# Kernel tuning notes

Measured on AMD Instinct MI355X. Metric: run time of the kernel, lower is better.

## Reference

```python
import jax, jax.numpy as jnp
import numpy as np
from jax import lax

T_STEPS = 40
BATCH = 2048
UNITS = 1024
INPUT_DIM = 1024
Q_BASIS = 8
ORDER = 4  # skfda BSpline default (cubic)


def bspline_basis(ts, q, k=ORDER):
    """Cox-de Boor B-spline basis, n_basis=q, order k, domain [0,1]. ts: (T,) -> (T,q)."""
    ts = np.asarray(ts, dtype=np.float64)
    breaks = np.linspace(0.0, 1.0, q - k + 2)
    knots = np.concatenate([np.zeros(k - 1), breaks, np.ones(k - 1)])  # len q+k
    n0 = len(knots) - 1
    N = np.zeros((len(ts), n0))
    for i in range(n0):
        N[:, i] = ((ts >= knots[i]) & (ts < knots[i + 1])).astype(np.float64)
    for d in range(1, k):
        Nn = np.zeros((len(ts), n0 - d))
        for i in range(n0 - d):
            out = np.zeros(len(ts))
            den1 = knots[i + d] - knots[i]
            if den1 > 0:
                out += (ts - knots[i]) / den1 * N[:, i]
            den2 = knots[i + d + 1] - knots[i + 1]
            if den2 > 0:
                out += (knots[i + d + 1] - ts) / den2 * N[:, i + 1]
            Nn[:, i] = out
        N = Nn
    # at right endpoint t==1 only the last basis is nonzero (value 1)
    at_end = ts >= 1.0 - 1e-12
    N[at_end] = 0.0
    N[at_end, -1] = 1.0
    return N.astype(np.float32)


def setup_inputs() -> dict:
    key = jax.random.key(0)
    k1, k2, k3 = jax.random.split(key, 3)
    D = UNITS + INPUT_DIM
    x = jax.random.normal(k1, (BATCH, T_STEPS, INPUT_DIM), dtype=jnp.float32)
    h0 = jnp.zeros((BATCH, UNITS), dtype=jnp.float32)
    Qw = jax.random.normal(k2, (D, Q_BASIS * UNITS), dtype=jnp.float32) / np.sqrt(D)
    bias = jax.random.uniform(k3, (UNITS,), dtype=jnp.float32, minval=-0.05, maxval=0.05)
    Bt_all = jnp.asarray(bspline_basis(np.linspace(0.0, 1.0, T_STEPS), Q_BASIS))
    return {"x": x, "h0": h0, "Qw": Qw, "bias": bias, "Bt_all": Bt_all}


def reference(x, h0, Qw, bias, Bt_all):
    B, T, I = x.shape
    U = h0.shape[-1]
    q = Bt_all.shape[-1]
    D = Qw.shape[0]
    # block_diag(Bt,...,Bt).T contraction == reshape Q to (D, U, q) and contract q with Bt
    Qr = Qw.reshape(D, U, q)
    W_all = jnp.einsum('duq,tq->tdu', Qr, Bt_all)  # (T, D, U) per-step weight matrices

    def step(h, xw):
        x_t, W_t = xw                       # (B,I), (D,U)
        cat = jnp.concatenate([h, x_t], axis=-1)  # (B, U+I) = (B, D); state first, as in cell
        h_new = jnp.tanh(cat @ W_t + bias)
        return h_new, h_new

    xs = jnp.swapaxes(x, 0, 1)              # (T, B, I)
    _, hs = lax.scan(step, h0, (xs, W_all))
    return jnp.swapaxes(hs, 0, 1)           # (B, T, U)
```

## Files before the change

### kernel.cpp

```cpp
#include <hip/hip_runtime.h>
#include <hip/hip_fp16.h>

#define TS 40
#define NB 2048
#define NU 1024
#define NI 1024
#define ND 2048
#define UD (1024 * 2048)

typedef _Float16 half8 __attribute__((ext_vector_type(8)));
typedef _Float16 half4v __attribute__((ext_vector_type(4)));
typedef float floatx4 __attribute__((ext_vector_type(4)));

__device__ __forceinline__ float tanh_fast(float v) {
  float e = __expf(2.0f * v);
  return 1.0f - 2.0f / (e + 1.0f);
}

__device__ __forceinline__ void gload16(const void* g, void* l) {
  __builtin_amdgcn_global_load_lds(
      (const __attribute__((address_space(1))) void*)g,
      (__attribute__((address_space(3))) void*)l, 16, 0, 0);
}

__device__ __forceinline__ int tile_off(int r, int c8) {
  return (((((r >> 4) * 2 + (c8 >> 2)) << 6) + ((c8 & 3) << 4) + (r & 15)) << 4);
}


__global__ __launch_bounds__(256) void prep_all(
    const float* __restrict__ Qw, const float* __restrict__ Bt,
    _Float16* __restrict__ W,
    const float* __restrict__ x, _Float16* __restrict__ X,
    const float* __restrict__ h0, _Float16* __restrict__ hb)
{
  __shared__ char shm[66816];
  const int tid = threadIdx.x;
  const int bid = blockIdx.x;

  if (bid < 512) {
    _Float16* ldsQ = (_Float16*)shm;
    float* ldsB = (float*)(shm + 65536);
    const int kt = bid & 31;
    const int ut = bid >> 5;
    for (int i = tid; i < TS * 8; i += 256) ldsB[i] = Bt[i];
    const float* qb = Qw + (size_t)(kt * 64) * 8192 + ut * 512;
#pragma unroll
    for (int i = 0; i < 32; ++i) {
      int s = i * 256 + tid;
      int dk = s >> 7, c4 = s & 127;
      float4 v = *(const float4*)(qb + (size_t)dk * 8192 + c4 * 4);
      _Float16* d = &ldsQ[dk * 512 + c4 * 4];
      d[0] = (_Float16)v.x; d[1] = (_Float16)v.y;
      d[2] = (_Float16)v.z; d[3] = (_Float16)v.w;
    }
    __syncthreads();
    const int w = tid >> 6, lane = tid & 63;
    const int dur = lane & 7, ko = lane >> 3;
#pragma unroll 1
    for (int sp = 0; sp < 2; ++sp) {
      const int stripe = w * 2 + sp;
      const int du = stripe * 8 + dur;
      float Q[8][8];
#pragma unroll
      for (int j = 0; j < 8; ++j)
#pragma unroll
        for (int q = 0; q < 8; ++q)
          Q[j][q] = (float)ldsQ[(ko * 8 + j) * 512 + du * 8 + q];
      const int obase = tile_off(du, ko);
#pragma unroll 1
      for (int t = 0; t < TS; ++t) {
        float b[8];
#pragma unroll
        for (int q = 0; q < 8; ++q) b[q] = ldsB[t * 8 + q];
        half8 v;
#pragma unroll
        for (int j = 0; j < 8; ++j) {
          float s = 0.f;
#pragma unroll
          for (int q = 0; q < 8; ++q) s += Q[j][q] * b[q];
          v[j] = (_Float16)s;
        }
        size_t tile = ((size_t)t * 16 + ut) * 32 + kt;
        *(half8*)((char*)W + tile * 8192 + obase) = v;
      }
    }
  } else if (bid < 1792) {
    char* stage = shm;
    const int b2 = bid - 512;
    const int bt = b2 & 31, t = b2 >> 5;
    char* outb = (char*)X + ((size_t)(t * 32 + bt) * 16) * 8192;
    const int r = tid >> 2, cq = tid & 3;
#pragma unroll 1
    for (int kt = 0; kt < 16; ++kt) {
      const float* src =
          x + (size_t)(bt * 64 + r) * (TS * NI) + (size_t)t * NI + kt * 64 + cq * 16;
      float4 a0 = *(const float4*)(src);
      float4 a1 = *(const float4*)(src + 4);
      float4 a2 = *(const float4*)(src + 8);
      float4 a3 = *(const float4*)(src + 12);
      half8 h0v, h1v;
      h0v[0] = (_Float16)a0.x; h0v[1] = (_Float16)a0.y;
      h0v[2] = (_Float16)a0.z; h0v[3] = (_Float16)a0.w;
      h0v[4] = (_Float16)a1.x; h0v[5] = (_Float16)a1.y;
      h0v[6] = (_Float16)a1.z; h0v[7] = (_Float16)a1.w;
      h1v[0] = (_Float16)a2.x; h1v[1] = (_Float16)a2.y;
      h1v[2] = (_Float16)a2.z; h1v[3] = (_Float16)a2.w;
      h1v[4] = (_Float16)a3.x; h1v[5] = (_Float16)a3.y;
      h1v[6] = (_Float16)a3.z; h1v[7] = (_Float16)a3.w;
      *(half8*)(stage + tile_off(r, cq * 2)) = h0v;
      *(half8*)(stage + tile_off(r, cq * 2 + 1)) = h1v;
      __syncthreads();
      uint4 v0 = *(const uint4*)(stage + tid * 32);
      uint4 v1 = *(const uint4*)(stage + tid * 32 + 16);
      *(uint4*)(outb + (size_t)kt * 8192 + tid * 32) = v0;
      *(uint4*)(outb + (size_t)kt * 8192 + tid * 32 + 16) = v1;
      __syncthreads();
    }
  } else {
    int g = (bid - 1792) * 256 + tid;
    int tile_id = g >> 9, rc = g & 511;
    int bt = tile_id >> 4, kt = tile_id & 15;
    int r = rc >> 3, c8 = rc & 7;
    const float* src = h0 + (size_t)(bt * 64 + r) * NU + kt * 64 + c8 * 8;
    float4 v0 = *(const float4*)src;
    float4 v1 = *(const float4*)(src + 4);
    half8 h;
    h[0] = (_Float16)v0.x; h[1] = (_Float16)v0.y;
    h[2] = (_Float16)v0.z; h[3] = (_Float16)v0.w;
    h[4] = (_Float16)v1.x; h[5] = (_Float16)v1.y;
    h[6] = (_Float16)v1.z; h[7] = (_Float16)v1.w;
    *(half8*)((char*)hb + (size_t)tile_id * 8192 + tile_off(r, c8)) = h;
  }
}

__global__ __launch_bounds__(256) void xproj4(
    const _Float16* __restrict__ X, const _Float16* __restrict__ W,
    const float* __restrict__ bias, _Float16* __restrict__ pre)
{
  __shared__ char lds[65536];
  const int tid = threadIdx.x;
  const int bt2 = blockIdx.x;
  const int ut2 = blockIdx.y;
  const int t   = blockIdx.z;
  const int lane = tid & 63, w = tid >> 6;
  const int wm2 = w >> 1, wn2 = w & 1;
  const int l15 = lane & 15, lk = lane >> 4;

  const char* Xb = (const char*)X + (((size_t)t * 32 + bt2 * 2) * 16) * 8192;
  const char* Wb = (const char*)W + (((size_t)t * 16 + ut2 * 2) * 32 + 16) * 8192;

  float bv[4];
#pragma unroll
  for (int nf = 0; nf < 4; ++nf)
    bv[nf] = bias[ut2 * 128 + wn2 * 64 + nf * 16 + l15];

  auto issue = [&](int p) {
    const char* src = (w < 2)
        ? Xb + (size_t)w * (16 * 8192) + (size_t)p * 8192
        : Wb + (size_t)(w - 2) * (32 * 8192) + (size_t)p * 8192;
    src += lane * 16;
    char* dst = lds + (p & 1) * 32768 + w * 8192;
#pragma unroll
    for (int i = 0; i < 8; ++i) gload16(src + i * 1024, dst + i * 1024);
  };

  floatx4 acc[4][4] = {};

  auto comp = [&](int p) {
    const char* pA = lds + (p & 1) * 32768 + wm2 * 8192;
    const char* pB = lds + (p & 1) * 32768 + 16384 + wn2 * 8192;
    __builtin_amdgcn_s_setprio(1);
#pragma unroll
    for (int kk = 0; kk < 2; ++kk) {
      half8 af[4], bf[4];
#pragma unroll
      for (int mf = 0; mf < 4; ++mf)
        af[mf] = *(const half8*)(pA + ((mf * 2 + kk) << 10) + lane * 16);
#pragma unroll
      for (int nf = 0; nf < 4; ++nf)
        bf[nf] = *(const half8*)(pB + ((nf * 2 + kk) << 10) + lane * 16);
#pragma unroll
      for (int mf = 0; mf < 4; ++mf)
#pragma unroll
        for (int nf = 0; nf < 4; ++nf)
          acc[mf][nf] = __builtin_amdgcn_mfma_f32_16x16x32_f16(
              af[mf], bf[nf], acc[mf][nf], 0, 0, 0);
    }
    __builtin_amdgcn_s_setprio(0);
  };

  issue(0);
#pragma unroll 1
  for (int p = 0; p < 16; ++p) {
    if (p + 1 < 16) {
      issue(p + 1);
      asm volatile("s_waitcnt vmcnt(8)" ::: "memory");
    } else {
      asm volatile("s_waitcnt vmcnt(0)" ::: "memory");
    }
    __builtin_amdgcn_s_barrier();
    comp(p);
    __builtin_amdgcn_s_barrier();
  }

  char* pbase = (char*)pre + (size_t)t * (512 * 8192);
  const int bidS = (bt2 * 2 + wm2) + 32 * (ut2 * 2 + wn2);
#pragma unroll
  for (int k = 0; k < 2; ++k)
#pragma unroll
    for (int nfp = 0; nfp < 4; ++nfp) {
      _Float16 hv[8];
#pragma unroll
      for (int j = 0; j < 4; ++j) {
        hv[j]     = (_Float16)(acc[2 * k][nfp][j] + bv[nfp]);
        hv[4 + j] = (_Float16)(acc[2 * k + 1][nfp][j] + bv[nfp]);
      }
      int wS = k * 4 + nfp;
      char* dst = pbase + ((size_t)bidS * 512 + wS * 64 + lane) * 16;
      *(uint4*)dst = ((const uint4*)hv)[0];
    }
}

__global__ __launch_bounds__(512) void serial6(
    const _Float16* __restrict__ Wh,
    const _Float16* __restrict__ pret,
    const _Float16* __restrict__ hprev,
    _Float16* __restrict__ hnext,
    float* __restrict__ outt)
{
  __shared__ uint4 lds4[4096];
  const int tid = threadIdx.x, bid = blockIdx.x;
  const int bt = bid & 31, ut = bid >> 5;
  const int bidS = bt + 32 * ut;
  const int lane = tid & 63, w = tid >> 6;
  const int wm = w >> 2, wn = w & 3;
  const int l15 = lane & 15, lk = lane >> 4;
  const int b0 = bt * 64, u0 = ut * 64;

  uint4 prv;
  {
    const uint4* pp = (const uint4*)((const char*)pret +
                                     ((size_t)bidS * 512 + tid) * 16);
    prv = pp[0];
  }

  const char* Hb = (const char*)hprev + (size_t)bt * 16 * 8192;
  const char* Wb = (const char*)Wh + (size_t)ut * 32 * 8192;

  auto issue = [&](int kt) {
    char* la = (char*)lds4 + (kt & 3) * 16384 + w * 2048;
    const char* g = (w < 4)
        ? Hb + (size_t)kt * 8192 + w * 2048 + lane * 16
        : Wb + (size_t)kt * 8192 + (w - 4) * 2048 + lane * 16;
    gload16(g, la);
    gload16(g + 1024, la + 1024);
  };

  floatx4 acc[2] = {};

  issue(0);
  issue(1);
  issue(2);
#pragma unroll 1
  for (int p = 0; p < 16; ++p) {
    if (p < 14)       asm volatile("s_waitcnt vmcnt(4)" ::: "memory");
    else if (p == 14) asm volatile("s_waitcnt vmcnt(2)" ::: "memory");
    else              asm volatile("s_waitcnt vmcnt(0)" ::: "memory");
    __builtin_amdgcn_s_barrier();
    if (p + 3 < 16) issue(p + 3);
    const char* pA = (const char*)lds4 + (p & 3) * 16384;
    const char* pB = pA + 8192;
    __builtin_amdgcn_s_setprio(1);
#pragma unroll
    for (int kk = 0; kk < 2; ++kk) {
      half8 af[2], bf;
#pragma unroll
      for (int mf = 0; mf < 2; ++mf)
        af[mf] = *(const half8*)(pA + ((((wm * 2 + mf) * 2 + kk) << 10) + lane * 16));
      bf = *(const half8*)(pB + (((wn * 2 + kk) << 10) + lane * 16));
#pragma unroll
      for (int mf = 0; mf < 2; ++mf)
        acc[mf] = __builtin_amdgcn_mfma_f32_16x16x32_f16(af[mf], bf, acc[mf], 0, 0, 0);
    }
    __builtin_amdgcn_s_setprio(0);
  }

  _Float16 prh[8];
  *(uint4*)&prh[0] = prv;
  {
    int u = u0 + wn * 16 + l15;
#pragma unroll
    for (int mf = 0; mf < 2; ++mf) {
      int brow = b0 + wm * 32 + mf * 16 + (lk << 2);
#pragma unroll
      for (int j = 0; j < 4; ++j) {
        int b = brow + j;
        float p = (float)prh[mf * 4 + j];
        float v = tanh_fast(acc[mf][j] + p);
        outt[(size_t)b * (TS * NU) + u] = v;
        *(_Float16*)((char*)hnext + (((size_t)(bt * 16 + ut)) << 13) +
                     tile_off(b & 63, (u & 63) >> 3) + (u & 7) * 2) = (_Float16)v;
      }
    }
  }
}

__global__ __launch_bounds__(256) void wprep_lin(
    const float* __restrict__ Qw, const float* __restrict__ Bt,
    _Float16* __restrict__ W, int t0, int nt)
{
  __shared__ float ldsQ[32 * 257];
  __shared__ float ldsB[TS * 8];
  const int tid = threadIdx.x;
  const int k0 = blockIdx.x * 32;
  const int u0 = blockIdx.y * 32;
  for (int i = tid; i < TS * 8; i += 256) ldsB[i] = Bt[i];
  const float* qbase = Qw + (size_t)k0 * 8192 + (size_t)u0 * 8;
#pragma unroll
  for (int i = 0; i < 8; ++i) {
    int s = i * 256 + tid;
    int r = s >> 6, c4 = s & 63;
    float4 v = *(const float4*)(qbase + (size_t)r * 8192 + c4 * 4);
    float* d = &ldsQ[r * 257 + c4 * 4];
    d[0] = v.x; d[1] = v.y; d[2] = v.z; d[3] = v.w;
  }
  __syncthreads();
  const int kl = tid & 31;
  const int ug = tid >> 5;
#pragma unroll
  for (int p = 0; p < 4; ++p) {
    int uu = p * 8 + ug;
    float q[8];
#pragma unroll
    for (int j = 0; j < 8; ++j) q[j] = ldsQ[kl * 257 + uu * 8 + j];
    size_t obase = (size_t)(u0 + uu) * 2048 + k0 + kl;
    for (int tt = 0; tt < nt; ++tt) {
      const float* bt = &ldsB[(t0 + tt) * 8];
      float v = 0.f;
#pragma unroll
      for (int j = 0; j < 8; ++j) v += q[j] * bt[j];
      W[(size_t)tt * UD + obase] = (_Float16)v;
    }
  }
}

__global__ __launch_bounds__(256) void step_gemm(
    const float* __restrict__ xt, const float* __restrict__ hp, long hstride,
    const _Float16* __restrict__ Wt, const float* __restrict__ bias,
    float* __restrict__ outt)
{
  __shared__ _Float16 ldsA[2][64 * 64];
  __shared__ _Float16 ldsB[2][128 * 64];
  const int tid = threadIdx.x;
  const int b0 = blockIdx.x * 64;
  const int u0 = blockIdx.y * 128;
  const int lane = tid & 63;
  const int wv = tid >> 6;
  const int wm = wv >> 1, wn = wv & 1;
  const int l15 = lane & 15, lk = lane >> 4;

  float4 areg[4];
  uint4 breg[4];

  auto stage_load = [&](int kt) {
    const int k0 = kt * 64;
    const float* src; size_t stride; int koff;
    if (k0 < NU) { src = hp; stride = (size_t)hstride; koff = k0; }
    else { src = xt; stride = (size_t)TS * NI; koff = k0 - NU; }
#pragma unroll
    for (int i = 0; i < 4; ++i) {
      int s = i * 256 + tid;
      int r = s >> 4, c4 = s & 15;
      areg[i] = *(const float4*)(src + (size_t)(b0 + r) * stride + koff + c4 * 4);
    }
    const _Float16* wsrc = Wt + (size_t)u0 * 2048 + k0;
#pragma unroll
    for (int i = 0; i < 4; ++i) {
      int s = i * 256 + tid;
      int u = s >> 3, c8 = s & 7;
      breg[i] = *(const uint4*)(wsrc + (size_t)u * 2048 + c8 * 8);
    }
  };

  auto stage_write = [&](int buf) {
    char* pA = (char*)&ldsA[buf][0];
    char* pB = (char*)&ldsB[buf][0];
#pragma unroll
    for (int i = 0; i < 4; ++i) {
      int s = i * 256 + tid;
      int r = s >> 4, c4 = s & 15;
      half4v h;
      h[0] = (_Float16)areg[i].x; h[1] = (_Float16)areg[i].y;
      h[2] = (_Float16)areg[i].z; h[3] = (_Float16)areg[i].w;
      int off = (r * 128 + c4 * 8) ^ ((r & 7) << 4);
      *(half4v*)(pA + off) = h;
    }
#pragma unroll
    for (int i = 0; i < 4; ++i) {
      int s = i * 256 + tid;
      int u = s >> 3, c8 = s & 7;
      int off = (u * 128 + c8 * 16) ^ ((u & 7) << 4);
      *(uint4*)(pB + off) = breg[i];
    }
  };

  floatx4 acc[2][4] = {};

  auto compute = [&](int buf) {
    const char* pA = (const char*)&ldsA[buf][0];
    const char* pB = (const char*)&ldsB[buf][0];
#pragma unroll
    for (int kk = 0; kk < 2; ++kk) {
      half8 af[2], bf[4];
#pragma unroll
      for (int mf = 0; mf < 2; ++mf) {
        int r = wm * 32 + mf * 16 + l15;
        int off = r * 128 + ((((kk << 2) | lk) ^ (r & 7)) << 4);
        af[mf] = *(const half8*)(pA + off);
      }
#pragma unroll
      for (int nf = 0; nf < 4; ++nf) {
        int u = wn * 64 + nf * 16 + l15;
        int off = u * 128 + ((((kk << 2) | lk) ^ (u & 7)) << 4);
        bf[nf] = *(const half8*)(pB + off);
      }
#pragma unroll
      for (int mf = 0; mf < 2; ++mf)
#pragma unroll
        for (int nf = 0; nf < 4; ++nf)
          acc[mf][nf] =
              __builtin_amdgcn_mfma_f32_16x16x32_f16(af[mf], bf[nf], acc[mf][nf], 0, 0, 0);
    }
  };

  stage_load(0);
  stage_write(0);
  __syncthreads();
#pragma unroll 1
  for (int kt = 0; kt < 32; ++kt) {
    int cur = kt & 1;
    if (kt + 1 < 32) stage_load(kt + 1);
    compute(cur);
    if (kt + 1 < 32) stage_write(cur ^ 1);
    __syncthreads();
  }

#pragma unroll
  for (int mf = 0; mf < 2; ++mf)
#pragma unroll
    for (int nf = 0; nf < 4; ++nf) {
      int u = u0 + wn * 64 + nf * 16 + l15;
      float bv = bias[u];
      int brow = b0 + wm * 32 + mf * 16 + (lk << 2);
#pragma unroll
      for (int j = 0; j < 4; ++j) {
        float prev = acc[mf][nf][j] + bv;
        outt[(size_t)(brow + j) * (TS * NU) + u] = tanh_fast(prev);
      }
    }
}

extern "C" void kernel_launch(void* const* d_in, const int* in_sizes, int n_in,
                              void* d_out, int out_size, void* d_ws, size_t ws_size,
                              hipStream_t stream) {
  const float* x    = (const float*)d_in[0];
  const float* h0   = (const float*)d_in[1];
  const float* Qw   = (const float*)d_in[2];
  const float* bias = (const float*)d_in[3];
  const float* Bt   = (const float*)d_in[4];
  float* out = (float*)d_out;

  char* ws = (char*)d_ws;
  const size_t w_bytes    = (size_t)UD * TS * sizeof(_Float16);
  const size_t x_bytes    = w_bytes;
  const size_t pre_bytes  = w_bytes;
  const size_t slot_bytes = (size_t)NB * NU * sizeof(_Float16);
  const size_t need = w_bytes + x_bytes + pre_bytes + 2 * slot_bytes;

  if (ws_size >= need) {
    _Float16* W   = (_Float16*)ws;
    _Float16* X   = (_Float16*)(ws + w_bytes);
    _Float16* pre = (_Float16*)(ws + w_bytes + x_bytes);
    _Float16* hb  = (_Float16*)(ws + w_bytes + x_bytes + pre_bytes);
    const size_t SLOT = (size_t)NB * NU;

    prep_all<<<dim3(2816), 256, 0, stream>>>(Qw, Bt, W, x, X, h0, hb);
    xproj4<<<dim3(16, 8, TS), 256, 0, stream>>>(X, W, bias, pre);

    for (int t = 0; t < TS; ++t) {
      const _Float16* hprev = hb + (size_t)(t & 1) * SLOT;
      _Float16* hnext = hb + (size_t)((t + 1) & 1) * SLOT;
      serial6<<<dim3(512), 512, 0, stream>>>(
          W + (size_t)t * UD, pre + (size_t)t * SLOT, hprev, hnext,
          out + (size_t)t * NU);
    }
  } else {
    _Float16* W = (_Float16*)ws;
    const bool big = ws_size >= w_bytes;
    if (big) wprep_lin<<<dim3(64, 32), 256, 0, stream>>>(Qw, Bt, W, 0, TS);
    for (int t = 0; t < TS; ++t) {
      const _Float16* Wtp;
      if (big) {
        Wtp = W + (size_t)t * UD;
      } else {
        wprep_lin<<<dim3(64, 32), 256, 0, stream>>>(Qw, Bt, W, t, 1);
        Wtp = W;
      }
      const float* hp = (t == 0) ? h0 : out + (size_t)(t - 1) * NU;
      long hstride = (t == 0) ? NU : (long)TS * NU;
      step_gemm<<<dim3(32, 8), 256, 0, stream>>>(
          x + (size_t)t * NI, hp, hstride, Wtp, bias, out + (size_t)t * NU);
    }
  }
}
```

Baseline: 922.2 us.

## Replace per-step serial kernel launches with one persistent cooperative kernel using flags

Swaps the 40 per-timestep serial6 launches for a single cooperative persistent kernel, serial7, that loops over time steps. Blocks synchronise through per-batch-tile atomic counters instead of kernel boundaries. Each block prefetches its weight tiles for the next step before spinning on the flag for the previous hidden state, so the weight loads overlap the wait. It removes launch gaps and lets tiles run ahead independently, but relies on co-residency of 512 blocks of 512 threads, falling back to the old loop if the cooperative launch fails.

```diff
diff --git a/kernel.cpp b/kernel.cpp
--- a/kernel.cpp
+++ b/kernel.cpp
@@ -32,7 +32,8 @@
     const float* __restrict__ Qw, const float* __restrict__ Bt,
     _Float16* __restrict__ W,
     const float* __restrict__ x, _Float16* __restrict__ X,
-    const float* __restrict__ h0, _Float16* __restrict__ hb)
+    const float* __restrict__ h0, _Float16* __restrict__ hb,
+    int* __restrict__ done)
 {
   __shared__ char shm[66816];
   const int tid = threadIdx.x;
@@ -117,7 +118,7 @@
       *(uint4*)(outb + (size_t)kt * 8192 + tid * 32 + 16) = v1;
       __syncthreads();
     }
-  } else {
+  } else if (bid < 2816) {
     int g = (bid - 1792) * 256 + tid;
     int tile_id = g >> 9, rc = g & 511;
     int bt = tile_id >> 4, kt = tile_id & 15;
@@ -131,6 +132,9 @@
     h[4] = (_Float16)v1.x; h[5] = (_Float16)v1.y;
     h[6] = (_Float16)v1.z; h[7] = (_Float16)v1.w;
     *(half8*)((char*)hb + (size_t)tile_id * 8192 + tile_off(r, c8)) = h;
+  } else {
+    for (int i = tid; i < TS * 32 / 4; i += 256)
+      ((int4*)done)[i] = make_int4(0, 0, 0, 0);
   }
 }
 
@@ -222,11 +226,120 @@
     }
 }
 
+__global__ __launch_bounds__(512) void serial7(
+    const _Float16* __restrict__ W, const _Float16* __restrict__ pre,
+    _Float16* __restrict__ hb, float* __restrict__ out,
+    int* __restrict__ done)
+{
+  __shared__ uint4 lds4[4096];
+  const size_t SLOT = (size_t)NB * NU;
+  const int tid = threadIdx.x, bid = blockIdx.x;
+  const int bt = bid & 31, ut = bid >> 5;
+  const int bidS = bt + 32 * ut;
+  const int lane = tid & 63, w = tid >> 6;
+  const int wm = w >> 2, wn = w & 3;
+  const int l15 = lane & 15, lk = lane >> 4;
+  const int b0 = bt * 64, u0 = ut * 64;
+
+#pragma unroll 1
+  for (int t = 0; t < TS; ++t) {
+    const char* Hb = (const char*)(hb + (size_t)(t & 1) * SLOT) +
+                     (size_t)bt * 16 * 8192;
+    _Float16* hnext = hb + (size_t)((t + 1) & 1) * SLOT;
+    const char* Wb = (const char*)(W + (size_t)t * UD) + (size_t)ut * 32 * 8192;
+    const _Float16* pret = pre + (size_t)t * SLOT;
+    float* outt = out + (size_t)t * NU;
+
+    uint4 prv = *(const uint4*)((const char*)pret +
+                                ((size_t)bidS * 512 + tid) * 16);
+
+    auto issueB = [&](int kt) {
+      if (w >= 4) {
+        char* la = (char*)lds4 + (kt & 3) * 16384 + w * 2048;
+        const char* g = Wb + (size_t)kt * 8192 + (w - 4) * 2048 + lane * 16;
+        gload16(g, la);
+        gload16(g + 1024, la + 1024);
+      }
+    };
+    auto issueA = [&](int kt) {
+      if (w < 4) {
+        char* la = (char*)lds4 + (kt & 3) * 16384 + w * 2048;
+        const char* g = Hb + (size_t)kt * 8192 + w * 2048 + lane * 16;
+        gload16(g, la);
+        gload16(g + 1024, la + 1024);
+      }
+    };
+
+    issueB(0); issueB(1); issueB(2);
+
+    if (t > 0) {
+      if (w == 0) {
+        const int* flag = &done[(t - 1) * 32 + bt];
+        int spins = 0;
+        while (__hip_atomic_load(flag, __ATOMIC_RELAXED,
+                                 __HIP_MEMORY_SCOPE_AGENT) < 16 &&
+               spins < (1 << 20)) ++spins;
+        (void)__hip_atomic_load(flag, __ATOMIC_ACQUIRE,
+                                __HIP_MEMORY_SCOPE_AGENT);
+      }
+      asm volatile("s_barrier" ::: "memory");
+    }
+    issueA(0); issueA(1); issueA(2);
+
+    floatx4 acc[2] = {};
+
+#pragma unroll 1
+    for (int p = 0; p < 16; ++p) {
+      if (p < 14)       asm volatile("s_waitcnt vmcnt(4)" ::: "memory");
+      else if (p == 14) asm volatile("s_waitcnt vmcnt(2)" ::: "memory");
+      else              asm volatile("s_waitcnt vmcnt(0)" ::: "memory");
+      __builtin_amdgcn_s_barrier();
+      if (p + 3 < 16) { issueA(p + 3); issueB(p + 3); }
+      const char* pA = (const char*)lds4 + (p & 3) * 16384;
+      const char* pB = pA + 8192;
+      __builtin_amdgcn_s_setprio(1);
+#pragma unroll
+      for (int kk = 0; kk < 2; ++kk) {
+        half8 af[2], bf;
+#pragma unroll
+        for (int mf = 0; mf < 2; ++mf)
+          af[mf] = *(const half8*)(pA + ((((wm * 2 + mf) * 2 + kk) << 10) + lane * 16));
+        bf = *(const half8*)(pB + (((wn * 2 + kk) << 10) + lane * 16));
+#pragma unroll
+        for (int mf = 0; mf < 2; ++mf)
+          acc[mf] = __builtin_amdgcn_mfma_f32_16x16x32_f16(af[mf], bf, acc[mf], 0, 0, 0);
+      }
+      __builtin_amdgcn_s_setprio(0);
+    }
+
+    _Float16 prh[8];
+    *(uint4*)&prh[0] = prv;
+    {
+      int u = u0 + wn * 16 + l15;
+#pragma unroll
+      for (int mf = 0; mf < 2; ++mf) {
+        int brow = b0 + wm * 32 + mf * 16 + (lk << 2);
+#pragma unroll
+        for (int j = 0; j < 4; ++j) {
+          int b = brow + j;
+          float p = (float)prh[mf * 4 + j];
+          float v = tanh_fast(acc[mf][j] + p);
+          outt[(size_t)b * (TS * NU) + u] = v;
+          *(_Float16*)((char*)hnext + (((size_t)(bt * 16 + ut)) << 13) +
+                       tile_off(b & 63, (u & 63) >> 3) + (u & 7) * 2) = (_Float16)v;
+        }
+      }
+    }
+    __syncthreads();
+    if (tid == 0)
+      __hip_atomic_fetch_add(&done[t * 32 + bt], 1, __ATOMIC_RELEASE,
+                             __HIP_MEMORY_SCOPE_AGENT);
+  }
+}
+
 __global__ __launch_bounds__(512) void serial6(
-    const _Float16* __restrict__ Wh,
-    const _Float16* __restrict__ pret,
-    const _Float16* __restrict__ hprev,
-    _Float16* __restrict__ hnext,
+    const _Float16* __restrict__ Wh, const _Float16* __restrict__ pret,
+    const _Float16* __restrict__ hprev, _Float16* __restrict__ hnext,
     float* __restrict__ outt)
 {
   __shared__ uint4 lds4[4096];
@@ -238,12 +351,8 @@
   const int l15 = lane & 15, lk = lane >> 4;
   const int b0 = bt * 64, u0 = ut * 64;
 
-  uint4 prv;
-  {
-    const uint4* pp = (const uint4*)((const char*)pret +
-                                     ((size_t)bidS * 512 + tid) * 16);
-    prv = pp[0];
-  }
+  uint4 prv = *(const uint4*)((const char*)pret +
+                              ((size_t)bidS * 512 + tid) * 16);
 
   const char* Hb = (const char*)hprev + (size_t)bt * 16 * 8192;
   const char* Wb = (const char*)Wh + (size_t)ut * 32 * 8192;
@@ -476,24 +585,37 @@
   const size_t x_bytes    = w_bytes;
   const size_t pre_bytes  = w_bytes;
   const size_t slot_bytes = (size_t)NB * NU * sizeof(_Float16);
-  const size_t need = w_bytes + x_bytes + pre_bytes + 2 * slot_bytes;
+  const size_t flag_bytes = (size_t)TS * 32 * sizeof(int);
+  const size_t need = w_bytes + x_bytes + pre_bytes + 2 * slot_bytes + flag_bytes;
 
   if (ws_size >= need) {
     _Float16* W   = (_Float16*)ws;
     _Float16* X   = (_Float16*)(ws + w_bytes);
     _Float16* pre = (_Float16*)(ws + w_bytes + x_bytes);
     _Float16* hb  = (_Float16*)(ws + w_bytes + x_bytes + pre_bytes);
+    int* done = (int*)(ws + w_bytes + x_bytes + pre_bytes + 2 * slot_bytes);
     const size_t SLOT = (size_t)NB * NU;
 
-    prep_all<<<dim3(2816), 256, 0, stream>>>(Qw, Bt, W, x, X, h0, hb);
+    prep_all<<<dim3(2817), 256, 0, stream>>>(Qw, Bt, W, x, X, h0, hb, done);
     xproj4<<<dim3(16, 8, TS), 256, 0, stream>>>(X, W, bias, pre);
 
-    for (int t = 0; t < TS; ++t) {
-      const _Float16* hprev = hb + (size_t)(t & 1) * SLOT;
-      _Float16* hnext = hb + (size_t)((t + 1) & 1) * SLOT;
-      serial6<<<dim3(512), 512, 0, stream>>>(
-          W + (size_t)t * UD, pre + (size_t)t * SLOT, hprev, hnext,
-          out + (size_t)t * NU);
+    const _Float16* Wa = W;
+    const _Float16* prea = pre;
+    _Float16* hba = hb;
+    float* outa = out;
+    int* donea = done;
+    void* args[5] = {(void*)&Wa, (void*)&prea, (void*)&hba, (void*)&outa,
+                     (void*)&donea};
+    hipError_t e = hipLaunchCooperativeKernel(
+        (const void*)serial7, dim3(512), dim3(512), args, 0, stream);
+    if (e != hipSuccess) {
+      for (int t = 0; t < TS; ++t) {
+        const _Float16* hprev = hb + (size_t)(t & 1) * SLOT;
+        _Float16* hnext = hb + (size_t)((t + 1) & 1) * SLOT;
+        serial6<<<dim3(512), 512, 0, stream>>>(
+            W + (size_t)t * UD, pre + (size_t)t * SLOT, hprev, hnext,
+            out + (size_t)t * NU);
+      }
     }
   } else {
     _Float16* W = (_Float16*)ws;
```

Measured after the change: 2.124 ms. 2.3x slower.
